# Kernel tuning notes

Measured on AMD Instinct MI355X. Metric: run time of the kernel, lower is better.

## Reference

```python
import jax, jax.numpy as jnp
import numpy as np

BETA = 0.25  # commitment loss weight


def setup_inputs() -> dict:
    key = jax.random.key(0)
    k1, k2 = jax.random.split(key)
    z = jax.random.normal(k1, (16, 64, 32, 32), dtype=jnp.float32)      # [B,C,H,W]
    emb = jax.random.normal(k2, (8192, 64), dtype=jnp.float32)          # [V,C] codebook
    return {"z": z, "emb": emb}


def reference(z, emb):
    b, c, h, w = z.shape
    # [B,C,H,W] -> [N,C] with N = B*H*W (channels-last flatten, as in torch permute+reshape)
    z_flat = jnp.transpose(z, (0, 2, 3, 1)).reshape(-1, c)
    # squared L2 distances to every code: ||z||^2 + ||e||^2 - 2 z.e
    dist = (
        jnp.sum(z_flat * z_flat, axis=1, keepdims=True)
        + jnp.sum(emb * emb, axis=1)
        - 2.0 * (z_flat @ emb.T)
    )  # [N,V]
    idx = jnp.argmin(dist, axis=1)  # [N]
    z_q = emb[idx].reshape(b, h, w, c).transpose(0, 3, 1, 2)  # [B,C,H,W]
    codebook_loss = jnp.mean((z_q - jax.lax.stop_gradient(z)) ** 2)
    commit_loss = jnp.mean((z - jax.lax.stop_gradient(z_q)) ** 2)
    vq_loss = codebook_loss + BETA * commit_loss
    # straight-through estimator
    z_q_st = z + jax.lax.stop_gradient(z_q - z)
    return z_q_st, idx.reshape(b, h, w), vq_loss
```

## Files before the change

kernel.cpp:

```cpp
#include <hip/hip_runtime.h>


typedef _Float16 half8 __attribute__((ext_vector_type(8)));
typedef float f32x4 __attribute__((ext_vector_type(4)));

#define N_PTS 16384
#define SPLITS 16
#define THR16 0.08f

__global__ __launch_bounds__(256) void k_pre(const float* __restrict__ emb,
                                             float* __restrict__ hneg,
                                             unsigned short* __restrict__ e16,
                                             float* __restrict__ embT,
                                             int* __restrict__ cnt) {
  int t = blockIdx.x * 256 + threadIdx.x;
  int v = t >> 2, part = t & 3;
  const float4* e4 = (const float4*)(emb + v * 64 + part * 16);
  float row[16];
  float s = 0.f;
#pragma unroll
  for (int i = 0; i < 4; ++i) {
    float4 a = e4[i];
    row[i * 4 + 0] = a.x; row[i * 4 + 1] = a.y;
    row[i * 4 + 2] = a.z; row[i * 4 + 3] = a.w;
    s += a.x * a.x + a.y * a.y + a.z * a.z + a.w * a.w;
  }
  s += __shfl_xor(s, 1);
  s += __shfl_xor(s, 2);
  unsigned short* base = e16 + (v >> 4) * 1024 + (v & 15) * 8;
#pragma unroll
  for (int g = 0; g < 2; ++g) {
    int c8 = part * 2 + g;
    half8 o;
#pragma unroll
    for (int j = 0; j < 8; ++j) o[j] = (_Float16)row[g * 8 + j];
    *(half8*)(base + (c8 >> 2) * 512 + (c8 & 3) * 128) = o;
  }
#pragma unroll
  for (int i = 0; i < 16; ++i) embT[(part * 16 + i) * 8192 + v] = row[i];
  if (part == 0) hneg[v] = -0.5f * s;
  if (t == 0) cnt[0] = 0;
}

__global__ __launch_bounds__(256, 3) void k1_score(
    const float* __restrict__ z, const unsigned short* __restrict__ e16,
    const float* __restrict__ hneg,
    float2* __restrict__ psp) {
  __shared__ float hs[512];
  const int tid = threadIdx.x;
  const int lane = tid & 63;
  const int wid = tid >> 6;
  const int cl = lane & 15;
  const int gq = lane >> 4;
  const int n0 = blockIdx.x * 256 + wid * 64;
  const int split = blockIdx.y;
  const int vbase = split * 512;

  *(float2*)&hs[tid * 2] = *(const float2*)(hneg + vbase + tid * 2);
  __syncthreads();

  const int b = n0 >> 10;
  const int hw0 = n0 & 1023;

  half8 A[4][2];
  {
    const float* zb = z + b * 65536 + hw0 + cl;
#pragma unroll
    for (int pt = 0; pt < 4; ++pt)
#pragma unroll
      for (int H = 0; H < 2; ++H) {
        half8 a;
#pragma unroll
        for (int j = 0; j < 8; ++j)
          a[j] = (_Float16)zb[pt * 16 + (H * 32 + gq * 8 + j) * 1024];
        A[pt][H] = a;
      }
  }

  float s1[4][4], s2[4][4];
#pragma unroll
  for (int pt = 0; pt < 4; ++pt)
#pragma unroll
    for (int r = 0; r < 4; ++r) { s1[pt][r] = -3.0e38f; s2[pt][r] = -3.0e38f; }

  const unsigned short* bp = e16 + vbase * 64 + lane * 8;
  int idxb = 8191 - (vbase + cl);

  half8 B0 = *(const half8*)bp;
  half8 B1 = *(const half8*)(bp + 512);

  for (int T = 0; T < 32; ++T) {
    half8 nB0, nB1;
    if (T < 31) {
      nB0 = *(const half8*)(bp + 1024);
      nB1 = *(const half8*)(bp + 1536);
    }
    const float nh = hs[T * 16 + cl];
    f32x4 C0;
    C0[0] = nh; C0[1] = nh; C0[2] = nh; C0[3] = nh;

#pragma unroll
    for (int pt = 0; pt < 4; ++pt) {
      f32x4 acc = __builtin_amdgcn_mfma_f32_16x16x32_f16(A[pt][0], B0, C0, 0, 0, 0);
      acc = __builtin_amdgcn_mfma_f32_16x16x32_f16(A[pt][1], B1, acc, 0, 0, 0);
#pragma unroll
      for (int r = 0; r < 4; ++r) {
        unsigned u = (__float_as_uint(acc[r]) & 0xFFFFE000u) | (unsigned)idxb;
        float p = __uint_as_float(u);
        s2[pt][r] = __builtin_amdgcn_fmed3f(p, s1[pt][r], s2[pt][r]);
        s1[pt][r] = fmaxf(s1[pt][r], p);
      }
    }
    idxb -= 16;
    B0 = nB0; B1 = nB1;
    bp += 1024;
  }

#pragma unroll
  for (int off = 8; off >= 1; off >>= 1) {
#pragma unroll
    for (int pt = 0; pt < 4; ++pt)
#pragma unroll
      for (int r = 0; r < 4; ++r) {
        float os = __shfl_xor(s1[pt][r], off);
        float o2 = __shfl_xor(s2[pt][r], off);
        s2[pt][r] = fmaxf(fmaxf(s2[pt][r], o2), fminf(s1[pt][r], os));
        s1[pt][r] = fmaxf(s1[pt][r], os);
      }
  }

  if (cl == 0) {
#pragma unroll
    for (int pt = 0; pt < 4; ++pt)
#pragma unroll
      for (int r = 0; r < 4; ++r) {
        int n = n0 + pt * 16 + gq * 4 + r;
        float2 o; o.x = s1[pt][r]; o.y = s2[pt][r];
        psp[split * N_PTS + n] = o;
      }
  }
}

__global__ __launch_bounds__(256) void k2_merge(
    const float2* __restrict__ psp,
    int* __restrict__ idxf, float* __restrict__ out_idx,
    int* __restrict__ list, int* __restrict__ cnt,
    unsigned long long* __restrict__ rpack, int* __restrict__ gdone) {
  int n = blockIdx.x * 256 + threadIdx.x;
  float S1 = -3.0e38f, S2 = -3.0e38f;
#pragma unroll
  for (int s = 0; s < SPLITS; ++s) {
    float2 a = psp[s * N_PTS + n];
    if (a.x > S1) { S2 = fmaxf(fmaxf(S2, a.y), S1); S1 = a.x; }
    else          { S2 = fmaxf(S2, a.x); }
  }
  int I1 = 8191 - (int)(__float_as_uint(S1) & 0x1FFFu);
  idxf[n] = I1;
  out_idx[n] = (float)I1;
  float q = fmaxf(fabsf(S1), fabsf(S2)) * 0.0009765625f;
  if (S1 - S2 < THR16 + q) {
    int p = atomicAdd(cnt, 1);
    list[p] = n;
    rpack[p] = 0ull;
    gdone[(p >> 3) * 16] = 0;
  }
}

__global__ __launch_bounds__(256, 4) void k_rescue(
    const float* __restrict__ z, const float* __restrict__ embT,
    const float* __restrict__ hneg, const int* __restrict__ list,
    const int* __restrict__ cnt, unsigned long long* __restrict__ rpack,
    int* __restrict__ gdone, int* __restrict__ idxf,
    float* __restrict__ out_idx) {
  __shared__ float zsT[64][8];
  __shared__ int pn[8];
  __shared__ unsigned long long red[4][8];
  __shared__ int lastS;
  const int tid = threadIdx.x;
  const int lane = tid & 63, wv = tid >> 6;
  const int count = *cnt;
  const int ntasks = ((count + 7) >> 3) << 3;

  for (int task = blockIdx.x; task < ntasks; task += gridDim.x) {
    const int grp = task >> 3, chunk = task & 7;
    const int base = grp * 8;
    const int P = min(8, count - base);
    __syncthreads();
    if (tid < 8) pn[tid] = list[base + min(tid, P - 1)];
    __syncthreads();
#pragma unroll
    for (int i = tid; i < 512; i += 256) {
      int p = i >> 6, c = i & 63;
      int n = pn[p];
      zsT[c][p] = z[(n >> 10) * 65536 + c * 1024 + (n & 1023)];
    }
    __syncthreads();

    float d[32];
#pragma unroll
    for (int i = 0; i < 32; ++i) d[i] = 0.f;

    const float4* ep = (const float4*)embT + chunk * 256 + tid;
    float4 cur = ep[0];
    for (int c = 0; c < 64; ++c) {
      float4 nxt;
      if (c < 63) nxt = ep[(c + 1) * 2048];
      float4 zpA = *(const float4*)&zsT[c][0];
      float4 zpB = *(const float4*)&zsT[c][4];
#pragma unroll
      for (int k = 0; k < 4; ++k) {
        float e = (k == 0) ? cur.x : (k == 1) ? cur.y : (k == 2) ? cur.z : cur.w;
        float* dp = d + k * 8;
        dp[0] = fmaf(e, zpA.x, dp[0]); dp[1] = fmaf(e, zpA.y, dp[1]);
        dp[2] = fmaf(e, zpA.z, dp[2]); dp[3] = fmaf(e, zpA.w, dp[3]);
        dp[4] = fmaf(e, zpB.x, dp[4]); dp[5] = fmaf(e, zpB.y, dp[5]);
        dp[6] = fmaf(e, zpB.z, dp[6]); dp[7] = fmaf(e, zpB.w, dp[7]);
      }
      if (c < 63) cur = nxt;
    }

    float4 hv = *(const float4*)(hneg + chunk * 1024 + tid * 4);
    unsigned long long best[8];
#pragma unroll
    for (int p = 0; p < 8; ++p) best[p] = 0ull;
#pragma unroll
    for (int k = 0; k < 4; ++k) {
      float hk = (k == 0) ? hv.x : (k == 1) ? hv.y : (k == 2) ? hv.z : hv.w;
      unsigned tag = (unsigned)(8191 - (chunk * 1024 + tid * 4 + k));
#pragma unroll
      for (int p = 0; p < 8; ++p) {
        float sc = d[k * 8 + p] + hk;
        unsigned u = __float_as_uint(sc);
        unsigned sb = (u & 0x80000000u) ? ~u : (u | 0x80000000u);
        unsigned long long pk = ((unsigned long long)sb << 32) | tag;
        best[p] = (pk > best[p]) ? pk : best[p];
      }
    }
#pragma unroll
    for (int off = 32; off >= 1; off >>= 1) {
#pragma unroll
      for (int p = 0; p < 8; ++p) {
        unsigned long long o = __shfl_xor(best[p], off);
        best[p] = (o > best[p]) ? o : best[p];
      }
    }
    if (lane == 0)
#pragma unroll
      for (int p = 0; p < 8; ++p) red[wv][p] = best[p];
    __syncthreads();
    if (tid < 8) {
      unsigned long long bmax = red[0][tid];
#pragma unroll
      for (int w = 1; w < 4; ++w) bmax = (red[w][tid] > bmax) ? red[w][tid] : bmax;
      if (tid < P) atomicMax(&rpack[base + tid], bmax);
    }
    __syncthreads();
    if (tid == 0) {
      lastS = (__hip_atomic_fetch_add(&gdone[grp * 16], 1, __ATOMIC_ACQ_REL,
                                      __HIP_MEMORY_SCOPE_AGENT) == 7) ? 1 : 0;
    }
    __syncthreads();
    if (lastS && tid < P) {
      unsigned long long pk = __hip_atomic_load(&rpack[base + tid],
                                                __ATOMIC_RELAXED,
                                                __HIP_MEMORY_SCOPE_AGENT);
      int code = 8191 - (int)(pk & 0xFFFFFFFFull);
      int n = pn[tid];
      idxf[n] = code;
      out_idx[n] = (float)code;
    }
  }
}

__global__ __launch_bounds__(256) void k3_quant(
    const float* __restrict__ z, const float* __restrict__ emb,
    const int* __restrict__ idxf,
    float* __restrict__ out, float* __restrict__ psum) {
  int t = blockIdx.x * 256 + threadIdx.x;
  int g = t * 4;
  int b = g >> 16;
  int c = (g >> 10) & 63;
  int hw = g & 1023;
  int n = (b << 10) | hw;
  float4 zv = *(const float4*)(z + g);
  int4 iv = *(const int4*)(idxf + n);
  float q0 = emb[iv.x * 64 + c];
  float q1 = emb[iv.y * 64 + c];
  float q2 = emb[iv.z * 64 + c];
  float q3 = emb[iv.w * 64 + c];
  float d0 = q0 - zv.x, d1 = q1 - zv.y, d2 = q2 - zv.z, d3 = q3 - zv.w;
  float4 o;
  o.x = zv.x + d0; o.y = zv.y + d1; o.z = zv.z + d2; o.w = zv.w + d3;
  *(float4*)(out + g) = o;
  float val = d0 * d0 + d1 * d1 + d2 * d2 + d3 * d3;
#pragma unroll
  for (int off = 32; off >= 1; off >>= 1) val += __shfl_down(val, off);
  __shared__ float wsum[4];
  int lane = threadIdx.x & 63, wv = threadIdx.x >> 6;
  if (lane == 0) wsum[wv] = val;
  __syncthreads();
  if (threadIdx.x == 0)
    psum[blockIdx.x] = wsum[0] + wsum[1] + wsum[2] + wsum[3];
}

__global__ __launch_bounds__(256) void k4_loss(const float* __restrict__ psum,
                                               float* __restrict__ out_loss) {
  int tid = threadIdx.x;
  float val = psum[tid] + psum[tid + 256] + psum[tid + 512] + psum[tid + 768];
#pragma unroll
  for (int off = 32; off >= 1; off >>= 1) val += __shfl_down(val, off);
  __shared__ float wsum[4];
  int lane = tid & 63, wv = tid >> 6;
  if (lane == 0) wsum[wv] = val;
  __syncthreads();
  if (tid == 0)
    out_loss[0] = 1.25f * (wsum[0] + wsum[1] + wsum[2] + wsum[3]) * (1.0f / 1048576.0f);
}

extern "C" void kernel_launch(void* const* d_in, const int* in_sizes, int n_in,
                              void* d_out, int out_size, void* d_ws, size_t ws_size,
                              hipStream_t stream) {
  const float* z   = (const float*)d_in[0];
  const float* emb = (const float*)d_in[1];
  float* out = (float*)d_out;
  float* ws  = (float*)d_ws;

  float* hneg = ws;
  unsigned short* e16 = (unsigned short*)(ws + 8192);
  float* embT = ws + 8192 + 262144;
  float2* psp = (float2*)(embT + 524288);
  int* idxf  = (int*)(psp + SPLITS * N_PTS);
  int* list  = idxf + N_PTS;
  int* cnt   = list + N_PTS;
  float* psum = (float*)(cnt + 4);
  unsigned long long* rpack = (unsigned long long*)(psum + 1024);
  int* gdone = (int*)(rpack + N_PTS);

  float* out_idx  = out + 1048576;
  float* out_loss = out + 1048576 + 16384;

  k_pre<<<128, 256, 0, stream>>>(emb, hneg, e16, embT, cnt);
  k1_score<<<dim3(64, SPLITS), 256, 0, stream>>>(z, e16, hneg, psp);
  k2_merge<<<64, 256, 0, stream>>>(psp, idxf, out_idx, list, cnt, rpack, gdone);
  k_rescue<<<1024, 256, 0, stream>>>(z, embT, hneg, list, cnt, rpack,
                                     gdone, idxf, out_idx);
  k3_quant<<<1024, 256, 0, stream>>>(z, emb, idxf, out, psum);
  k4_loss<<<1, 256, 0, stream>>>(psum, out_loss);
}
```

Baseline: 141.5 us.

## Fuse all VQ stages into one persistent kernel with grid-wide barriers

Replaces six separate kernel launches with a single persistent kernel of 512 blocks that uses atomic-counter grid barriers between the preprocess, scoring, merge, rescue and quantize/loss phases. Scoring now runs two codebook splits per block to fit the smaller grid, and the final loss reduction is done by block 0 after a completion counter. Counters and the rescue scratch buffers are zeroed by one memset instead of being reset inside the kernels. This removes launch gaps and per-kernel tail effects, but it relies on all 512 blocks being co-resident and adds spin-barrier overhead. The scoring phase also has fewer blocks than before.

```diff
diff --git a/kernel.cpp b/kernel.cpp
--- a/kernel.cpp
+++ b/kernel.cpp
@@ -7,314 +7,336 @@
 #define N_PTS 16384
 #define SPLITS 16
 #define THR16 0.08f
-
-__global__ __launch_bounds__(256) void k_pre(const float* __restrict__ emb,
-                                             float* __restrict__ hneg,
-                                             unsigned short* __restrict__ e16,
-                                             float* __restrict__ embT,
-                                             int* __restrict__ cnt) {
-  int t = blockIdx.x * 256 + threadIdx.x;
-  int v = t >> 2, part = t & 3;
-  const float4* e4 = (const float4*)(emb + v * 64 + part * 16);
-  float row[16];
-  float s = 0.f;
-#pragma unroll
-  for (int i = 0; i < 4; ++i) {
-    float4 a = e4[i];
-    row[i * 4 + 0] = a.x; row[i * 4 + 1] = a.y;
-    row[i * 4 + 2] = a.z; row[i * 4 + 3] = a.w;
-    s += a.x * a.x + a.y * a.y + a.z * a.z + a.w * a.w;
-  }
-  s += __shfl_xor(s, 1);
-  s += __shfl_xor(s, 2);
-  unsigned short* base = e16 + (v >> 4) * 1024 + (v & 15) * 8;
-#pragma unroll
-  for (int g = 0; g < 2; ++g) {
-    int c8 = part * 2 + g;
-    half8 o;
-#pragma unroll
-    for (int j = 0; j < 8; ++j) o[j] = (_Float16)row[g * 8 + j];
-    *(half8*)(base + (c8 >> 2) * 512 + (c8 & 3) * 128) = o;
-  }
-#pragma unroll
-  for (int i = 0; i < 16; ++i) embT[(part * 16 + i) * 8192 + v] = row[i];
-  if (part == 0) hneg[v] = -0.5f * s;
-  if (t == 0) cnt[0] = 0;
+#define GRID 512
+
+__device__ __forceinline__ void dbar(int* ctr) {
+  __syncthreads();
+  if (threadIdx.x == 0) {
+    __threadfence();
+    __hip_atomic_fetch_add(ctr, 1, __ATOMIC_RELEASE, __HIP_MEMORY_SCOPE_AGENT);
+    while (__hip_atomic_load(ctr, __ATOMIC_ACQUIRE, __HIP_MEMORY_SCOPE_AGENT) < GRID)
+      __builtin_amdgcn_s_sleep(32);
+  }
+  __syncthreads();
 }
 
-__global__ __launch_bounds__(256, 3) void k1_score(
-    const float* __restrict__ z, const unsigned short* __restrict__ e16,
-    const float* __restrict__ hneg,
-    float2* __restrict__ psp) {
+__global__ __launch_bounds__(256, 4) void k_fused(
+    const float* __restrict__ z, const float* __restrict__ emb,
+    float* __restrict__ out, float* __restrict__ hneg,
+    unsigned short* __restrict__ e16, float* __restrict__ embT,
+    float2* __restrict__ psp, int* __restrict__ idxf, int* __restrict__ list,
+    unsigned long long* __restrict__ rpack, int* __restrict__ gdone,
+    float* __restrict__ psum, int* __restrict__ ctrs,
+    float* __restrict__ out_idx, float* __restrict__ out_loss) {
   __shared__ float hs[512];
-  const int tid = threadIdx.x;
-  const int lane = tid & 63;
-  const int wid = tid >> 6;
-  const int cl = lane & 15;
-  const int gq = lane >> 4;
-  const int n0 = blockIdx.x * 256 + wid * 64;
-  const int split = blockIdx.y;
-  const int vbase = split * 512;
-
-  *(float2*)&hs[tid * 2] = *(const float2*)(hneg + vbase + tid * 2);
-  __syncthreads();
-
-  const int b = n0 >> 10;
-  const int hw0 = n0 & 1023;
-
-  half8 A[4][2];
-  {
-    const float* zb = z + b * 65536 + hw0 + cl;
-#pragma unroll
-    for (int pt = 0; pt < 4; ++pt)
-#pragma unroll
-      for (int H = 0; H < 2; ++H) {
-        half8 a;
-#pragma unroll
-        for (int j = 0; j < 8; ++j)
-          a[j] = (_Float16)zb[pt * 16 + (H * 32 + gq * 8 + j) * 1024];
-        A[pt][H] = a;
-      }
-  }
-
-  float s1[4][4], s2[4][4];
-#pragma unroll
-  for (int pt = 0; pt < 4; ++pt)
-#pragma unroll
-    for (int r = 0; r < 4; ++r) { s1[pt][r] = -3.0e38f; s2[pt][r] = -3.0e38f; }
-
-  const unsigned short* bp = e16 + vbase * 64 + lane * 8;
-  int idxb = 8191 - (vbase + cl);
-
-  half8 B0 = *(const half8*)bp;
-  half8 B1 = *(const half8*)(bp + 512);
-
-  for (int T = 0; T < 32; ++T) {
-    half8 nB0, nB1;
-    if (T < 31) {
-      nB0 = *(const half8*)(bp + 1024);
-      nB1 = *(const half8*)(bp + 1536);
-    }
-    const float nh = hs[T * 16 + cl];
-    f32x4 C0;
-    C0[0] = nh; C0[1] = nh; C0[2] = nh; C0[3] = nh;
-
-#pragma unroll
-    for (int pt = 0; pt < 4; ++pt) {
-      f32x4 acc = __builtin_amdgcn_mfma_f32_16x16x32_f16(A[pt][0], B0, C0, 0, 0, 0);
-      acc = __builtin_amdgcn_mfma_f32_16x16x32_f16(A[pt][1], B1, acc, 0, 0, 0);
-#pragma unroll
-      for (int r = 0; r < 4; ++r) {
-        unsigned u = (__float_as_uint(acc[r]) & 0xFFFFE000u) | (unsigned)idxb;
-        float p = __uint_as_float(u);
-        s2[pt][r] = __builtin_amdgcn_fmed3f(p, s1[pt][r], s2[pt][r]);
-        s1[pt][r] = fmaxf(s1[pt][r], p);
-      }
-    }
-    idxb -= 16;
-    B0 = nB0; B1 = nB1;
-    bp += 1024;
-  }
-
-#pragma unroll
-  for (int off = 8; off >= 1; off >>= 1) {
-#pragma unroll
-    for (int pt = 0; pt < 4; ++pt)
-#pragma unroll
-      for (int r = 0; r < 4; ++r) {
-        float os = __shfl_xor(s1[pt][r], off);
-        float o2 = __shfl_xor(s2[pt][r], off);
-        s2[pt][r] = fmaxf(fmaxf(s2[pt][r], o2), fminf(s1[pt][r], os));
-        s1[pt][r] = fmaxf(s1[pt][r], os);
-      }
-  }
-
-  if (cl == 0) {
-#pragma unroll
-    for (int pt = 0; pt < 4; ++pt)
-#pragma unroll
-      for (int r = 0; r < 4; ++r) {
-        int n = n0 + pt * 16 + gq * 4 + r;
-        float2 o; o.x = s1[pt][r]; o.y = s2[pt][r];
-        psp[split * N_PTS + n] = o;
-      }
-  }
-}
-
-__global__ __launch_bounds__(256) void k2_merge(
-    const float2* __restrict__ psp,
-    int* __restrict__ idxf, float* __restrict__ out_idx,
-    int* __restrict__ list, int* __restrict__ cnt,
-    unsigned long long* __restrict__ rpack, int* __restrict__ gdone) {
-  int n = blockIdx.x * 256 + threadIdx.x;
-  float S1 = -3.0e38f, S2 = -3.0e38f;
-#pragma unroll
-  for (int s = 0; s < SPLITS; ++s) {
-    float2 a = psp[s * N_PTS + n];
-    if (a.x > S1) { S2 = fmaxf(fmaxf(S2, a.y), S1); S1 = a.x; }
-    else          { S2 = fmaxf(S2, a.x); }
-  }
-  int I1 = 8191 - (int)(__float_as_uint(S1) & 0x1FFFu);
-  idxf[n] = I1;
-  out_idx[n] = (float)I1;
-  float q = fmaxf(fabsf(S1), fabsf(S2)) * 0.0009765625f;
-  if (S1 - S2 < THR16 + q) {
-    int p = atomicAdd(cnt, 1);
-    list[p] = n;
-    rpack[p] = 0ull;
-    gdone[(p >> 3) * 16] = 0;
-  }
-}
-
-__global__ __launch_bounds__(256, 4) void k_rescue(
-    const float* __restrict__ z, const float* __restrict__ embT,
-    const float* __restrict__ hneg, const int* __restrict__ list,
-    const int* __restrict__ cnt, unsigned long long* __restrict__ rpack,
-    int* __restrict__ gdone, int* __restrict__ idxf,
-    float* __restrict__ out_idx) {
   __shared__ float zsT[64][8];
   __shared__ int pn[8];
   __shared__ unsigned long long red[4][8];
   __shared__ int lastS;
+  __shared__ float wsum[4];
+
   const int tid = threadIdx.x;
-  const int lane = tid & 63, wv = tid >> 6;
-  const int count = *cnt;
-  const int ntasks = ((count + 7) >> 3) << 3;
-
-  for (int task = blockIdx.x; task < ntasks; task += gridDim.x) {
-    const int grp = task >> 3, chunk = task & 7;
-    const int base = grp * 8;
-    const int P = min(8, count - base);
-    __syncthreads();
-    if (tid < 8) pn[tid] = list[base + min(tid, P - 1)];
-    __syncthreads();
-#pragma unroll
-    for (int i = tid; i < 512; i += 256) {
-      int p = i >> 6, c = i & 63;
-      int n = pn[p];
-      zsT[c][p] = z[(n >> 10) * 65536 + c * 1024 + (n & 1023)];
-    }
-    __syncthreads();
-
-    float d[32];
-#pragma unroll
-    for (int i = 0; i < 32; ++i) d[i] = 0.f;
-
-    const float4* ep = (const float4*)embT + chunk * 256 + tid;
-    float4 cur = ep[0];
-    for (int c = 0; c < 64; ++c) {
-      float4 nxt;
-      if (c < 63) nxt = ep[(c + 1) * 2048];
-      float4 zpA = *(const float4*)&zsT[c][0];
-      float4 zpB = *(const float4*)&zsT[c][4];
+  const int lane = tid & 63;
+  const int wid = tid >> 6;
+  const int bid = blockIdx.x;
+
+  if (bid < 128) {
+    int t = bid * 256 + tid;
+    int v = t >> 2, part = t & 3;
+    const float4* e4 = (const float4*)(emb + v * 64 + part * 16);
+    float row[16];
+    float s = 0.f;
+#pragma unroll
+    for (int i = 0; i < 4; ++i) {
+      float4 a = e4[i];
+      row[i * 4 + 0] = a.x; row[i * 4 + 1] = a.y;
+      row[i * 4 + 2] = a.z; row[i * 4 + 3] = a.w;
+      s += a.x * a.x + a.y * a.y + a.z * a.z + a.w * a.w;
+    }
+    s += __shfl_xor(s, 1);
+    s += __shfl_xor(s, 2);
+    unsigned short* base = e16 + (v >> 4) * 1024 + (v & 15) * 8;
+#pragma unroll
+    for (int g = 0; g < 2; ++g) {
+      int c8 = part * 2 + g;
+      half8 o;
+#pragma unroll
+      for (int j = 0; j < 8; ++j) o[j] = (_Float16)row[g * 8 + j];
+      *(half8*)(base + (c8 >> 2) * 512 + (c8 & 3) * 128) = o;
+    }
+#pragma unroll
+    for (int i = 0; i < 16; ++i) embT[(part * 16 + i) * 8192 + v] = row[i];
+    if (part == 0) hneg[v] = -0.5f * s;
+  }
+  dbar(ctrs + 1);
+
+  {
+    const int bx = bid & 63;
+    const int sb = bid >> 6;
+    const int cl = lane & 15;
+    const int gq = lane >> 4;
+    const int n0 = bx * 256 + wid * 64;
+    const int b = n0 >> 10;
+    const int hw0 = n0 & 1023;
+
+    half8 A[4][2];
+    {
+      const float* zb = z + b * 65536 + hw0 + cl;
+#pragma unroll
+      for (int pt = 0; pt < 4; ++pt)
+#pragma unroll
+        for (int H = 0; H < 2; ++H) {
+          half8 a;
+#pragma unroll
+          for (int j = 0; j < 8; ++j)
+            a[j] = (_Float16)zb[pt * 16 + (H * 32 + gq * 8 + j) * 1024];
+          A[pt][H] = a;
+        }
+    }
+
+    for (int sp = 0; sp < 2; ++sp) {
+      const int split = sb + sp * 8;
+      const int vbase = split * 512;
+      __syncthreads();
+      *(float2*)&hs[tid * 2] = *(const float2*)(hneg + vbase + tid * 2);
+      __syncthreads();
+
+      float s1[4][4], s2[4][4];
+#pragma unroll
+      for (int pt = 0; pt < 4; ++pt)
+#pragma unroll
+        for (int r = 0; r < 4; ++r) { s1[pt][r] = -3.0e38f; s2[pt][r] = -3.0e38f; }
+
+      const unsigned short* bp = e16 + vbase * 64 + lane * 8;
+      int idxb = 8191 - (vbase + cl);
+
+      half8 B0 = *(const half8*)bp;
+      half8 B1 = *(const half8*)(bp + 512);
+
+      for (int T = 0; T < 32; ++T) {
+        half8 nB0, nB1;
+        if (T < 31) {
+          nB0 = *(const half8*)(bp + 1024);
+          nB1 = *(const half8*)(bp + 1536);
+        }
+        const float nh = hs[T * 16 + cl];
+        f32x4 C0;
+        C0[0] = nh; C0[1] = nh; C0[2] = nh; C0[3] = nh;
+
+#pragma unroll
+        for (int pt = 0; pt < 4; ++pt) {
+          f32x4 acc = __builtin_amdgcn_mfma_f32_16x16x32_f16(A[pt][0], B0, C0, 0, 0, 0);
+          acc = __builtin_amdgcn_mfma_f32_16x16x32_f16(A[pt][1], B1, acc, 0, 0, 0);
+#pragma unroll
+          for (int r = 0; r < 4; ++r) {
+            unsigned u = (__float_as_uint(acc[r]) & 0xFFFFE000u) | (unsigned)idxb;
+            float p = __uint_as_float(u);
+            s2[pt][r] = __builtin_amdgcn_fmed3f(p, s1[pt][r], s2[pt][r]);
+            s1[pt][r] = fmaxf(s1[pt][r], p);
+          }
+        }
+        idxb -= 16;
+        B0 = nB0; B1 = nB1;
+        bp += 1024;
+      }
+
+#pragma unroll
+      for (int off = 8; off >= 1; off >>= 1) {
+#pragma unroll
+        for (int pt = 0; pt < 4; ++pt)
+#pragma unroll
+          for (int r = 0; r < 4; ++r) {
+            float os = __shfl_xor(s1[pt][r], off);
+            float o2 = __shfl_xor(s2[pt][r], off);
+            s2[pt][r] = fmaxf(fmaxf(s2[pt][r], o2), fminf(s1[pt][r], os));
+            s1[pt][r] = fmaxf(s1[pt][r], os);
+          }
+      }
+
+      if (cl == 0) {
+#pragma unroll
+        for (int pt = 0; pt < 4; ++pt)
+#pragma unroll
+          for (int r = 0; r < 4; ++r) {
+            int n = n0 + pt * 16 + gq * 4 + r;
+            float2 o; o.x = s1[pt][r]; o.y = s2[pt][r];
+            psp[split * N_PTS + n] = o;
+          }
+      }
+    }
+  }
+  dbar(ctrs + 2);
+
+  if (tid < 32) {
+    int n = bid * 32 + tid;
+    float S1 = -3.0e38f, S2 = -3.0e38f;
+#pragma unroll
+    for (int s = 0; s < SPLITS; ++s) {
+      float2 a = psp[s * N_PTS + n];
+      if (a.x > S1) { S2 = fmaxf(fmaxf(S2, a.y), S1); S1 = a.x; }
+      else          { S2 = fmaxf(S2, a.x); }
+    }
+    int I1 = 8191 - (int)(__float_as_uint(S1) & 0x1FFFu);
+    idxf[n] = I1;
+    out_idx[n] = (float)I1;
+    float q = fmaxf(fabsf(S1), fabsf(S2)) * 0.0009765625f;
+    if (S1 - S2 < THR16 + q) {
+      int p = __hip_atomic_fetch_add(ctrs, 1, __ATOMIC_RELAXED,
+                                     __HIP_MEMORY_SCOPE_AGENT);
+      list[p] = n;
+    }
+  }
+  dbar(ctrs + 3);
+
+  {
+    const int count = __hip_atomic_load(ctrs, __ATOMIC_RELAXED,
+                                        __HIP_MEMORY_SCOPE_AGENT);
+    const int ntasks = ((count + 7) >> 3) << 3;
+
+    for (int task = bid; task < ntasks; task += GRID) {
+      const int grp = task >> 3, chunk = task & 7;
+      const int base = grp * 8;
+      const int P = min(8, count - base);
+      __syncthreads();
+      if (tid < 8) pn[tid] = list[base + min(tid, P - 1)];
+      __syncthreads();
+#pragma unroll
+      for (int i = tid; i < 512; i += 256) {
+        int p = i >> 6, c = i & 63;
+        int n = pn[p];
+        zsT[c][p] = z[(n >> 10) * 65536 + c * 1024 + (n & 1023)];
+      }
+      __syncthreads();
+
+      float d[32];
+#pragma unroll
+      for (int i = 0; i < 32; ++i) d[i] = 0.f;
+
+      const float4* ep = (const float4*)embT + chunk * 256 + tid;
+      float4 cur = ep[0];
+      for (int c = 0; c < 64; ++c) {
+        float4 nxt;
+        if (c < 63) nxt = ep[(c + 1) * 2048];
+        float4 zpA = *(const float4*)&zsT[c][0];
+        float4 zpB = *(const float4*)&zsT[c][4];
+#pragma unroll
+        for (int k = 0; k < 4; ++k) {
+          float e = (k == 0) ? cur.x : (k == 1) ? cur.y : (k == 2) ? cur.z : cur.w;
+          float* dp = d + k * 8;
+          dp[0] = fmaf(e, zpA.x, dp[0]); dp[1] = fmaf(e, zpA.y, dp[1]);
+          dp[2] = fmaf(e, zpA.z, dp[2]); dp[3] = fmaf(e, zpA.w, dp[3]);
+          dp[4] = fmaf(e, zpB.x, dp[4]); dp[5] = fmaf(e, zpB.y, dp[5]);
+          dp[6] = fmaf(e, zpB.z, dp[6]); dp[7] = fmaf(e, zpB.w, dp[7]);
+        }
+        if (c < 63) cur = nxt;
+      }
+
+      float4 hv = *(const float4*)(hneg + chunk * 1024 + tid * 4);
+      unsigned long long best[8];
+#pragma unroll
+      for (int p = 0; p < 8; ++p) best[p] = 0ull;
 #pragma unroll
       for (int k = 0; k < 4; ++k) {
-        float e = (k == 0) ? cur.x : (k == 1) ? cur.y : (k == 2) ? cur.z : cur.w;
-        float* dp = d + k * 8;
-        dp[0] = fmaf(e, zpA.x, dp[0]); dp[1] = fmaf(e, zpA.y, dp[1]);
-        dp[2] = fmaf(e, zpA.z, dp[2]); dp[3] = fmaf(e, zpA.w, dp[3]);
-        dp[4] = fmaf(e, zpB.x, dp[4]); dp[5] = fmaf(e, zpB.y, dp[5]);
-        dp[6] = fmaf(e, zpB.z, dp[6]); dp[7] = fmaf(e, zpB.w, dp[7]);
-      }
-      if (c < 63) cur = nxt;
-    }
-
-    float4 hv = *(const float4*)(hneg + chunk * 1024 + tid * 4);
-    unsigned long long best[8];
-#pragma unroll
-    for (int p = 0; p < 8; ++p) best[p] = 0ull;
-#pragma unroll
-    for (int k = 0; k < 4; ++k) {
-      float hk = (k == 0) ? hv.x : (k == 1) ? hv.y : (k == 2) ? hv.z : hv.w;
-      unsigned tag = (unsigned)(8191 - (chunk * 1024 + tid * 4 + k));
-#pragma unroll
-      for (int p = 0; p < 8; ++p) {
-        float sc = d[k * 8 + p] + hk;
-        unsigned u = __float_as_uint(sc);
-        unsigned sb = (u & 0x80000000u) ? ~u : (u | 0x80000000u);
-        unsigned long long pk = ((unsigned long long)sb << 32) | tag;
-        best[p] = (pk > best[p]) ? pk : best[p];
-      }
-    }
-#pragma unroll
-    for (int off = 32; off >= 1; off >>= 1) {
-#pragma unroll
-      for (int p = 0; p < 8; ++p) {
-        unsigned long long o = __shfl_xor(best[p], off);
-        best[p] = (o > best[p]) ? o : best[p];
-      }
-    }
-    if (lane == 0)
-#pragma unroll
-      for (int p = 0; p < 8; ++p) red[wv][p] = best[p];
-    __syncthreads();
-    if (tid < 8) {
-      unsigned long long bmax = red[0][tid];
-#pragma unroll
-      for (int w = 1; w < 4; ++w) bmax = (red[w][tid] > bmax) ? red[w][tid] : bmax;
-      if (tid < P) atomicMax(&rpack[base + tid], bmax);
-    }
-    __syncthreads();
+        float hk = (k == 0) ? hv.x : (k == 1) ? hv.y : (k == 2) ? hv.z : hv.w;
+        unsigned tag = (unsigned)(8191 - (chunk * 1024 + tid * 4 + k));
+#pragma unroll
+        for (int p = 0; p < 8; ++p) {
+          float sc = d[k * 8 + p] + hk;
+          unsigned u = __float_as_uint(sc);
+          unsigned sb2 = (u & 0x80000000u) ? ~u : (u | 0x80000000u);
+          unsigned long long pk = ((unsigned long long)sb2 << 32) | tag;
+          best[p] = (pk > best[p]) ? pk : best[p];
+        }
+      }
+#pragma unroll
+      for (int off = 32; off >= 1; off >>= 1) {
+#pragma unroll
+        for (int p = 0; p < 8; ++p) {
+          unsigned long long o = __shfl_xor(best[p], off);
+          best[p] = (o > best[p]) ? o : best[p];
+        }
+      }
+      if (lane == 0)
+#pragma unroll
+        for (int p = 0; p < 8; ++p) red[wid][p] = best[p];
+      __syncthreads();
+      if (tid < 8) {
+        unsigned long long bmax = red[0][tid];
+#pragma unroll
+        for (int w = 1; w < 4; ++w) bmax = (red[w][tid] > bmax) ? red[w][tid] : bmax;
+        if (tid < P) atomicMax(&rpack[base + tid], bmax);
+      }
+      __syncthreads();
+      if (tid == 0) {
+        lastS = (__hip_atomic_fetch_add(&gdone[grp * 16], 1, __ATOMIC_ACQ_REL,
+                                        __HIP_MEMORY_SCOPE_AGENT) == 7) ? 1 : 0;
+      }
+      __syncthreads();
+      if (lastS && tid < P) {
+        unsigned long long pk = __hip_atomic_load(&rpack[base + tid],
+                                                  __ATOMIC_RELAXED,
+                                                  __HIP_MEMORY_SCOPE_AGENT);
+        int code = 8191 - (int)(pk & 0xFFFFFFFFull);
+        int n = pn[tid];
+        idxf[n] = code;
+        out_idx[n] = (float)code;
+      }
+    }
+  }
+  dbar(ctrs + 4);
+
+  {
+    float val = 0.f;
+#pragma unroll
+    for (int it = 0; it < 2; ++it) {
+      int t = it * 131072 + bid * 256 + tid;
+      int g = t * 4;
+      int b = g >> 16;
+      int c = (g >> 10) & 63;
+      int hw = g & 1023;
+      int n = (b << 10) | hw;
+      float4 zv = *(const float4*)(z + g);
+      int4 iv = *(const int4*)(idxf + n);
+      float q0 = emb[iv.x * 64 + c];
+      float q1 = emb[iv.y * 64 + c];
+      float q2 = emb[iv.z * 64 + c];
+      float q3 = emb[iv.w * 64 + c];
+      float d0 = q0 - zv.x, d1 = q1 - zv.y, d2 = q2 - zv.z, d3 = q3 - zv.w;
+      float4 o;
+      o.x = zv.x + d0; o.y = zv.y + d1; o.z = zv.z + d2; o.w = zv.w + d3;
+      *(float4*)(out + g) = o;
+      val += d0 * d0 + d1 * d1 + d2 * d2 + d3 * d3;
+    }
+#pragma unroll
+    for (int off = 32; off >= 1; off >>= 1) val += __shfl_down(val, off);
+    __syncthreads();
+    if (lane == 0) wsum[wid] = val;
+    __syncthreads();
+    if (tid == 0)
+      psum[bid] = wsum[0] + wsum[1] + wsum[2] + wsum[3];
+  }
+
+  __syncthreads();
+  if (tid == 0) {
+    __threadfence();
+    __hip_atomic_fetch_add(ctrs + 5, 1, __ATOMIC_RELEASE, __HIP_MEMORY_SCOPE_AGENT);
+  }
+  if (bid == 0) {
     if (tid == 0) {
-      lastS = (__hip_atomic_fetch_add(&gdone[grp * 16], 1, __ATOMIC_ACQ_REL,
-                                      __HIP_MEMORY_SCOPE_AGENT) == 7) ? 1 : 0;
-    }
-    __syncthreads();
-    if (lastS && tid < P) {
-      unsigned long long pk = __hip_atomic_load(&rpack[base + tid],
-                                                __ATOMIC_RELAXED,
-                                                __HIP_MEMORY_SCOPE_AGENT);
-      int code = 8191 - (int)(pk & 0xFFFFFFFFull);
-      int n = pn[tid];
-      idxf[n] = code;
-      out_idx[n] = (float)code;
-    }
-  }
-}
-
-__global__ __launch_bounds__(256) void k3_quant(
-    const float* __restrict__ z, const float* __restrict__ emb,
-    const int* __restrict__ idxf,
-    float* __restrict__ out, float* __restrict__ psum) {
-  int t = blockIdx.x * 256 + threadIdx.x;
-  int g = t * 4;
-  int b = g >> 16;
-  int c = (g >> 10) & 63;
-  int hw = g & 1023;
-  int n = (b << 10) | hw;
-  float4 zv = *(const float4*)(z + g);
-  int4 iv = *(const int4*)(idxf + n);
-  float q0 = emb[iv.x * 64 + c];
-  float q1 = emb[iv.y * 64 + c];
-  float q2 = emb[iv.z * 64 + c];
-  float q3 = emb[iv.w * 64 + c];
-  float d0 = q0 - zv.x, d1 = q1 - zv.y, d2 = q2 - zv.z, d3 = q3 - zv.w;
-  float4 o;
-  o.x = zv.x + d0; o.y = zv.y + d1; o.z = zv.z + d2; o.w = zv.w + d3;
-  *(float4*)(out + g) = o;
-  float val = d0 * d0 + d1 * d1 + d2 * d2 + d3 * d3;
-#pragma unroll
-  for (int off = 32; off >= 1; off >>= 1) val += __shfl_down(val, off);
-  __shared__ float wsum[4];
-  int lane = threadIdx.x & 63, wv = threadIdx.x >> 6;
-  if (lane == 0) wsum[wv] = val;
-  __syncthreads();
-  if (threadIdx.x == 0)
-    psum[blockIdx.x] = wsum[0] + wsum[1] + wsum[2] + wsum[3];
-}
-
-__global__ __launch_bounds__(256) void k4_loss(const float* __restrict__ psum,
-                                               float* __restrict__ out_loss) {
-  int tid = threadIdx.x;
-  float val = psum[tid] + psum[tid + 256] + psum[tid + 512] + psum[tid + 768];
-#pragma unroll
-  for (int off = 32; off >= 1; off >>= 1) val += __shfl_down(val, off);
-  __shared__ float wsum[4];
-  int lane = tid & 63, wv = tid >> 6;
-  if (lane == 0) wsum[wv] = val;
-  __syncthreads();
-  if (tid == 0)
-    out_loss[0] = 1.25f * (wsum[0] + wsum[1] + wsum[2] + wsum[3]) * (1.0f / 1048576.0f);
+      while (__hip_atomic_load(ctrs + 5, __ATOMIC_ACQUIRE,
+                               __HIP_MEMORY_SCOPE_AGENT) < GRID)
+        __builtin_amdgcn_s_sleep(32);
+    }
+    __syncthreads();
+    float v = psum[tid] + psum[tid + 256];
+#pragma unroll
+    for (int off = 32; off >= 1; off >>= 1) v += __shfl_down(v, off);
+    __syncthreads();
+    if (lane == 0) wsum[wid] = v;
+    __syncthreads();
+    if (tid == 0)
+      out_loss[0] = 1.25f * (wsum[0] + wsum[1] + wsum[2] + wsum[3]) * (1.0f / 1048576.0f);
+  }
 }
 
 extern "C" void kernel_launch(void* const* d_in, const int* in_sizes, int n_in,
@@ -331,19 +353,18 @@
   float2* psp = (float2*)(embT + 524288);
   int* idxf  = (int*)(psp + SPLITS * N_PTS);
   int* list  = idxf + N_PTS;
-  int* cnt   = list + N_PTS;
-  float* psum = (float*)(cnt + 4);
-  unsigned long long* rpack = (unsigned long long*)(psum + 1024);
+  float* psum = (float*)(list + N_PTS);
+  int* ctrs  = (int*)(psum + 512);
+  unsigned long long* rpack = (unsigned long long*)(ctrs + 16);
   int* gdone = (int*)(rpack + N_PTS);
 
   float* out_idx  = out + 1048576;
   float* out_loss = out + 1048576 + 16384;
 
-  k_pre<<<128, 256, 0, stream>>>(emb, hneg, e16, embT, cnt);
-  k1_score<<<dim3(64, SPLITS), 256, 0, stream>>>(z, e16, hneg, psp);
-  k2_merge<<<64, 256, 0, stream>>>(psp, idxf, out_idx, list, cnt, rpack, gdone);
-  k_rescue<<<1024, 256, 0, stream>>>(z, embT, hneg, list, cnt, rpack,
-                                     gdone, idxf, out_idx);
-  k3_quant<<<1024, 256, 0, stream>>>(z, emb, idxf, out, psum);
-  k4_loss<<<1, 256, 0, stream>>>(psum, out_loss);
+  size_t zbytes = 16 * 4 + (size_t)N_PTS * 8 + 2048 * 16 * 4;
+  (void)hipMemsetAsync(ctrs, 0, zbytes, stream);
+
+  k_fused<<<GRID, 256, 0, stream>>>(z, emb, out, hneg, e16, embT, psp, idxf,
+                                    list, rpack, gdone, psum, ctrs,
+                                    out_idx, out_loss);
 }
```

New measurement: 452.0 us. +219.4%, slower.
